# Performance work log

Measured on AMD Instinct MI355X. Metric: run time of the kernel, lower is better.

Reference implementation:

```python
import jax, jax.numpy as jnp
import numpy as np

EPS = 1e-6  # AllReduceParams default eps


def setup_inputs() -> dict:
    key = jax.random.key(0)
    k1, k2, k3, k4 = jax.random.split(key, 4)
    TP, T, H = 4, 8192, 4096
    return {
        "x_ranks": jax.random.normal(k1, (TP, T, H), dtype=jnp.float32) * 0.1,
        "residual": jax.random.normal(k2, (T, H), dtype=jnp.float32),
        "bias": jax.random.normal(k3, (H,), dtype=jnp.float32) * 0.01,
        "norm_weight": jax.random.uniform(k4, (H,), dtype=jnp.float32, minval=0.5, maxval=1.5),
    }


def reference(x_ranks, residual, bias, norm_weight):
    # Simulated allreduce: sum per-rank partial activations [TP, T, H] -> [T, H]
    reduced = jnp.sum(x_ranks, axis=0)
    # Fused RESIDUAL_RMS_NORM epilogue: bias add + residual add -> intermediate,
    # then RMSNorm with affine weight on the intermediate.
    inter = reduced + bias + residual  # [T, H] (returned as residual output)
    var = jnp.mean(jnp.square(inter), axis=-1, keepdims=True)
    norm = inter * jax.lax.rsqrt(var + EPS) * norm_weight
    return norm, inter
```

## Files before the change

### kernel.cpp

```cpp
#include <hip/hip_runtime.h>

#define TP_ 4
#define T_  8192
#define H_  4096
#define EPS_ 1e-6f

__global__ __launch_bounds__(256) void allreduce_rmsnorm_kernel(
    const float* __restrict__ x_ranks,
    const float* __restrict__ residual,
    const float* __restrict__ bias,
    const float* __restrict__ norm_weight,
    float* __restrict__ out_norm,
    float* __restrict__ out_inter)
{
    const int row = blockIdx.x;
    const int tid = threadIdx.x;
    const size_t row_off = (size_t)row * H_;
    const size_t rank_stride = (size_t)T_ * H_;

    const float4* __restrict__ r0  = (const float4*)(x_ranks + row_off);
    const float4* __restrict__ r1  = (const float4*)(x_ranks + rank_stride     + row_off);
    const float4* __restrict__ r2  = (const float4*)(x_ranks + rank_stride * 2 + row_off);
    const float4* __restrict__ r3  = (const float4*)(x_ranks + rank_stride * 3 + row_off);
    const float4* __restrict__ res = (const float4*)(residual + row_off);
    const float4* __restrict__ b4  = (const float4*)bias;
    const float4* __restrict__ w4  = (const float4*)norm_weight;

    float4 inter[4];
    float ss = 0.0f;

    #pragma unroll
    for (int c = 0; c < 4; ++c) {
        const int idx = c * 256 + tid;
        float4 a  = r0[idx];
        float4 b  = r1[idx];
        float4 cc = r2[idx];
        float4 d  = r3[idx];
        float4 rr = res[idx];
        float4 bb = b4[idx];
        float4 v;
        v.x = a.x + b.x + cc.x + d.x + bb.x + rr.x;
        v.y = a.y + b.y + cc.y + d.y + bb.y + rr.y;
        v.z = a.z + b.z + cc.z + d.z + bb.z + rr.z;
        v.w = a.w + b.w + cc.w + d.w + bb.w + rr.w;
        inter[c] = v;
        ss += v.x * v.x + v.y * v.y + v.z * v.z + v.w * v.w;
    }

    #pragma unroll
    for (int o = 32; o > 0; o >>= 1)
        ss += __shfl_down(ss, o, 64);

    __shared__ float s_partial[4];
    __shared__ float s_scale;
    const int lane = tid & 63;
    const int wave = tid >> 6;
    if (lane == 0) s_partial[wave] = ss;
    __syncthreads();
    if (tid == 0) {
        float tot = s_partial[0] + s_partial[1] + s_partial[2] + s_partial[3];
        s_scale = rsqrtf(tot * (1.0f / (float)H_) + EPS_);
    }
    __syncthreads();
    const float scale = s_scale;

    float4* __restrict__ on = (float4*)(out_norm + row_off);
    float4* __restrict__ oi = (float4*)(out_inter + row_off);

    #pragma unroll
    for (int c = 0; c < 4; ++c) {
        const int idx = c * 256 + tid;
        float4 v = inter[c];
        oi[idx] = v;
        float4 w = w4[idx];
        float4 n;
        n.x = v.x * scale * w.x;
        n.y = v.y * scale * w.y;
        n.z = v.z * scale * w.z;
        n.w = v.w * scale * w.w;
        on[idx] = n;
    }
}

extern "C" void kernel_launch(void* const* d_in, const int* in_sizes, int n_in,
                              void* d_out, int out_size, void* d_ws, size_t ws_size,
                              hipStream_t stream) {
    const float* x_ranks     = (const float*)d_in[0];
    const float* residual    = (const float*)d_in[1];
    const float* bias        = (const float*)d_in[2];
    const float* norm_weight = (const float*)d_in[3];

    float* out_norm  = (float*)d_out;
    float* out_inter = (float*)d_out + (size_t)T_ * H_;

    dim3 grid(T_);
    dim3 block(256);
    allreduce_rmsnorm_kernel<<<grid, block, 0, stream>>>(
        x_ranks, residual, bias, norm_weight, out_norm, out_inter);
}
```

Baseline: 832.0 us.

## Map one wavefront per row with nontemporal loads/stores and shuffle-only reduction

Each 64-lane wavefront now handles a full row, with 16 float4 chunks per lane. This removes the shared-memory and __syncthreads block reduction in favour of an xor-shuffle allreduce. Streaming inputs and both outputs go through nontemporal loads and stores to reduce cache pollution, and the intermediate is written early in the first pass. Register use per thread rises to 16 float4 values, which may lower occupancy and hurt latency hiding on this bandwidth-bound kernel.

Result: no change. 819.7 us (-1.5%).

```diff
diff --git a/kernel.cpp b/kernel.cpp
--- a/kernel.cpp
+++ b/kernel.cpp
@@ -4,6 +4,8 @@
 #define T_  8192
 #define H_  4096
 #define EPS_ 1e-6f
+
+typedef float f4 __attribute__((ext_vector_type(4)));
 
 __global__ __launch_bounds__(256) void allreduce_rmsnorm_kernel(
     const float* __restrict__ x_ranks,
@@ -13,72 +15,53 @@
     float* __restrict__ out_norm,
     float* __restrict__ out_inter)
 {
-    const int row = blockIdx.x;
-    const int tid = threadIdx.x;
+    const int lane = threadIdx.x & 63;
+    const int wave = threadIdx.x >> 6;
+    const int row  = blockIdx.x * 4 + wave;
     const size_t row_off = (size_t)row * H_;
     const size_t rank_stride = (size_t)T_ * H_;
 
-    const float4* __restrict__ r0  = (const float4*)(x_ranks + row_off);
-    const float4* __restrict__ r1  = (const float4*)(x_ranks + rank_stride     + row_off);
-    const float4* __restrict__ r2  = (const float4*)(x_ranks + rank_stride * 2 + row_off);
-    const float4* __restrict__ r3  = (const float4*)(x_ranks + rank_stride * 3 + row_off);
-    const float4* __restrict__ res = (const float4*)(residual + row_off);
-    const float4* __restrict__ b4  = (const float4*)bias;
-    const float4* __restrict__ w4  = (const float4*)norm_weight;
+    const f4* __restrict__ r0 = (const f4*)(x_ranks + row_off);
+    const f4* __restrict__ r1 = (const f4*)(x_ranks + rank_stride     + row_off);
+    const f4* __restrict__ r2 = (const f4*)(x_ranks + rank_stride * 2 + row_off);
+    const f4* __restrict__ r3 = (const f4*)(x_ranks + rank_stride * 3 + row_off);
+    const f4* __restrict__ re = (const f4*)(residual + row_off);
+    const f4* __restrict__ bb = (const f4*)bias;
+    const f4* __restrict__ ww = (const f4*)norm_weight;
+    f4* __restrict__ oi = (f4*)(out_inter + row_off);
+    f4* __restrict__ on = (f4*)(out_norm + row_off);
 
-    float4 inter[4];
+    f4 inter[16];
     float ss = 0.0f;
 
     #pragma unroll
-    for (int c = 0; c < 4; ++c) {
-        const int idx = c * 256 + tid;
-        float4 a  = r0[idx];
-        float4 b  = r1[idx];
-        float4 cc = r2[idx];
-        float4 d  = r3[idx];
-        float4 rr = res[idx];
-        float4 bb = b4[idx];
-        float4 v;
-        v.x = a.x + b.x + cc.x + d.x + bb.x + rr.x;
-        v.y = a.y + b.y + cc.y + d.y + bb.y + rr.y;
-        v.z = a.z + b.z + cc.z + d.z + bb.z + rr.z;
-        v.w = a.w + b.w + cc.w + d.w + bb.w + rr.w;
+    for (int c = 0; c < 16; ++c) {
+        const int idx = c * 64 + lane;
+        f4 a0 = __builtin_nontemporal_load(r0 + idx);
+        f4 a1 = __builtin_nontemporal_load(r1 + idx);
+        f4 a2 = __builtin_nontemporal_load(r2 + idx);
+        f4 a3 = __builtin_nontemporal_load(r3 + idx);
+        f4 rr = __builtin_nontemporal_load(re + idx);
+        f4 bv = bb[idx];
+        f4 v = a0 + a1 + a2 + a3 + bv + rr;
         inter[c] = v;
+        __builtin_nontemporal_store(v, oi + idx);
         ss += v.x * v.x + v.y * v.y + v.z * v.z + v.w * v.w;
     }
 
     #pragma unroll
-    for (int o = 32; o > 0; o >>= 1)
-        ss += __shfl_down(ss, o, 64);
+    for (int o = 1; o < 64; o <<= 1)
+        ss += __shfl_xor(ss, o, 64);
 
-    __shared__ float s_partial[4];
-    __shared__ float s_scale;
-    const int lane = tid & 63;
-    const int wave = tid >> 6;
-    if (lane == 0) s_partial[wave] = ss;
-    __syncthreads();
-    if (tid == 0) {
-        float tot = s_partial[0] + s_partial[1] + s_partial[2] + s_partial[3];
-        s_scale = rsqrtf(tot * (1.0f / (float)H_) + EPS_);
-    }
-    __syncthreads();
-    const float scale = s_scale;
-
-    float4* __restrict__ on = (float4*)(out_norm + row_off);
-    float4* __restrict__ oi = (float4*)(out_inter + row_off);
+    const float scale = rsqrtf(ss * (1.0f / (float)H_) + EPS_);
 
     #pragma unroll
-    for (int c = 0; c < 4; ++c) {
-        const int idx = c * 256 + tid;
-        float4 v = inter[c];
-        oi[idx] = v;
-        float4 w = w4[idx];
-        float4 n;
-        n.x = v.x * scale * w.x;
-        n.y = v.y * scale * w.y;
-        n.z = v.z * scale * w.z;
-        n.w = v.w * scale * w.w;
-        on[idx] = n;
+    for (int c = 0; c < 16; ++c) {
+        const int idx = c * 64 + lane;
+        f4 w = ww[idx];
+        f4 n = inter[c] * w;
+        n *= scale;
+        __builtin_nontemporal_store(n, on + idx);
     }
 }
 
@@ -93,7 +76,7 @@
     float* out_norm  = (float*)d_out;
     float* out_inter = (float*)d_out + (size_t)T_ * H_;
 
-    dim3 grid(T_);
+    dim3 grid(T_ / 4);
     dim3 block(256);
     allreduce_rmsnorm_kernel<<<grid, block, 0, stream>>>(
         x_ranks, residual, bias, norm_weight, out_norm, out_inter);
```
